# Optimization experiments

Measured on AMD Instinct MI355X. Metric: run time of the kernel, lower is better.

The kernel has to match this reference:

```python
import jax, jax.numpy as jnp
import numpy as np

TAU = 1.0 / 30.0
EPS = 1e-12  # matches torch F.normalize clamp_min eps


def _l2norm(x):
    n = jnp.sqrt(jnp.sum(x * x, axis=-1, keepdims=True))
    return x / jnp.maximum(n, EPS)


def setup_inputs() -> dict:
    key = jax.random.key(0)
    ks = jax.random.split(key, 6)
    L, B, D, KD = 4096, 4, 512, 128
    query = jax.random.normal(ks[0], (L, B, D), dtype=jnp.float32)
    k_in = jax.random.normal(ks[1], (L, B, D), dtype=jnp.float32)
    value = jax.random.normal(ks[2], (L, B, D), dtype=jnp.float32)
    # init: normal(0, sqrt(2/out_features)), zero bias
    WK_w = jax.random.normal(ks[3], (KD, D), dtype=jnp.float32) * np.sqrt(2.0 / KD)
    WK_b = jnp.zeros((KD,), dtype=jnp.float32)
    WV_w = jax.random.normal(ks[4], (D, D), dtype=jnp.float32) * np.sqrt(2.0 / D)
    WV_b = jnp.zeros((D,), dtype=jnp.float32)
    return {"query": query, "key": k_in, "value": value,
            "WK_w": WK_w, "WK_b": WK_b, "WV_w": WV_w, "WV_b": WV_b}


def reference(query, key, value, WK_w, WK_b, WV_w, WV_b):
    # query/key/value: [L, B, D]
    wk = _l2norm(key @ WK_w.T + WK_b)      # [Lk, B, KD]
    wq = _l2norm(query @ WK_w.T + WK_b)    # [Lq, B, KD]
    wv = value @ WV_w.T + WV_b             # [Lk, B, D]
    # cosine-similarity scores: [B, Lq, Lk]
    scores = jnp.einsum('qbk,sbk->bqs', wq, wk)
    affinity = jax.nn.softmax(scores / TAU, axis=-1)
    out = jnp.einsum('bqs,sbd->qbd', affinity, wv)  # [Lq, B, D]
    return out
```

## Files before the change

kernel.cpp:

```cpp
#include <hip/hip_runtime.h>

using bf16x8 = __attribute__((ext_vector_type(8))) short;
using u16x8  = __attribute__((ext_vector_type(8))) unsigned short;
using f32x4  = __attribute__((ext_vector_type(4))) float;
using f32x4v = __attribute__((ext_vector_type(4))) float;

__device__ inline unsigned short f2bf(float f) {
  unsigned int u = __builtin_bit_cast(unsigned int, f);
  return (unsigned short)((u + 0x7fffu + ((u >> 16) & 1u)) >> 16);
}

#define MFMA16(a, b, c) __builtin_amdgcn_mfma_f32_16x16x32_bf16((a), (b), (c), 0, 0, 0)

__device__ __forceinline__ void lds_barrier() {
  __builtin_amdgcn_sched_barrier(0);
  asm volatile("s_waitcnt lgkmcnt(0)" ::: "memory");
  __builtin_amdgcn_sched_barrier(0);
  __builtin_amdgcn_s_barrier();
  __builtin_amdgcn_sched_barrier(0);
}

#define LL 4096
#define NB 4
#define DD 512
#define KDIM 128

__device__ __forceinline__ void proj_qk_body(
    char* smem, int bid, const float* __restrict__ Xq, const float* __restrict__ Xk,
    const float* __restrict__ Wk, const float* __restrict__ bk,
    unsigned short* __restrict__ Outq, unsigned short* __restrict__ Outk)
{
  char* Xs = smem;
  char* Ws = smem + 16384;

  const int tid = threadIdx.x;
  const int w = tid >> 6, lane = tid & 63, lr = lane & 15, g = lane >> 4;
  const int sel = bid & 1;
  const float* X = sel ? Xk : Xq;
  unsigned short* Out = sel ? Outk : Outq;
  const int r0 = (bid >> 1) * 64;

  f32x4 acc[8];
  #pragma unroll
  for (int nt = 0; nt < 8; ++nt) acc[nt] = f32x4{0.f, 0.f, 0.f, 0.f};

  for (int kc = 0; kc < 4; ++kc) {
    if (kc) __syncthreads();
    #pragma unroll
    for (int p = 0; p < 4; ++p) {
      int j = tid + p * 256;
      int row = j >> 4, e0 = (j & 15) * 8;
      const float* src = X + (size_t)(r0 + row) * DD + kc * 128 + e0;
      f32x4v f0 = *reinterpret_cast<const f32x4v*>(src);
      f32x4v f1 = *reinterpret_cast<const f32x4v*>(src + 4);
      u16x8 v;
      #pragma unroll
      for (int e = 0; e < 4; ++e) { v[e] = f2bf(f0[e]); v[e + 4] = f2bf(f1[e]); }
      *reinterpret_cast<u16x8*>(Xs + row * 256 + ((e0 * 2) ^ ((row & 7) << 4))) = v;
    }
    #pragma unroll
    for (int p = 0; p < 8; ++p) {
      int j = tid + p * 256;
      int n = j >> 4, e0 = (j & 15) * 8;
      const float* src = Wk + (size_t)n * DD + kc * 128 + e0;
      f32x4v f0 = *reinterpret_cast<const f32x4v*>(src);
      f32x4v f1 = *reinterpret_cast<const f32x4v*>(src + 4);
      u16x8 v;
      #pragma unroll
      for (int e = 0; e < 4; ++e) { v[e] = f2bf(f0[e]); v[e + 4] = f2bf(f1[e]); }
      *reinterpret_cast<u16x8*>(Ws + n * 256 + ((e0 * 2) ^ ((n & 7) << 4))) = v;
    }
    __syncthreads();
    const int arow = w * 16 + lr;
    #pragma unroll
    for (int ks = 0; ks < 4; ++ks) {
      int oa = (ks * 64 + g * 16) ^ ((arow & 7) << 4);
      bf16x8 a = *reinterpret_cast<const bf16x8*>(Xs + arow * 256 + oa);
      #pragma unroll
      for (int nt = 0; nt < 8; ++nt) {
        int n = nt * 16 + lr;
        int ob = (ks * 64 + g * 16) ^ ((n & 7) << 4);
        bf16x8 bb = *reinterpret_cast<const bf16x8*>(Ws + n * 256 + ob);
        acc[nt] = MFMA16(a, bb, acc[nt]);
      }
    }
  }

  float bias[8];
  #pragma unroll
  for (int nt = 0; nt < 8; ++nt) bias[nt] = bk[nt * 16 + lr];
  #pragma unroll
  for (int nt = 0; nt < 8; ++nt)
    #pragma unroll
    for (int i = 0; i < 4; ++i) acc[nt][i] += bias[nt];

  f32x4 ss = f32x4{0.f, 0.f, 0.f, 0.f};
  #pragma unroll
  for (int nt = 0; nt < 8; ++nt)
    #pragma unroll
    for (int i = 0; i < 4; ++i) ss[i] += acc[nt][i] * acc[nt][i];
  #pragma unroll
  for (int m = 1; m < 16; m <<= 1) {
    #pragma unroll
    for (int i = 0; i < 4; ++i) ss[i] += __shfl_xor(ss[i], m);
  }
  float inv[4];
  #pragma unroll
  for (int i = 0; i < 4; ++i) inv[i] = 1.0f / fmaxf(sqrtf(ss[i]), 1e-12f);

  #pragma unroll
  for (int nt = 0; nt < 8; ++nt) {
    int c = nt * 16 + lr;
    #pragma unroll
    for (int i = 0; i < 4; ++i) {
      int r = r0 + w * 16 + g * 4 + i;
      int l = r >> 2, b = r & 3;
      Out[((size_t)(b * LL + l)) * KDIM + c] = f2bf(acc[nt][i] * inv[i]);
    }
  }
}

__device__ __forceinline__ void proj_v_body(
    char* smem, int bid, const float* __restrict__ X,
    const float* __restrict__ Wv, const float* __restrict__ bv,
    unsigned short* __restrict__ VtOut)
{
  char* Xs = smem;
  char* Ws = smem + 32768;

  const int tid = threadIdx.x;
  const int w = tid >> 6, lane = tid & 63, lr = lane & 15, g = lane >> 4;
  const int rb = bid >> 3, nb = bid & 7;
  const int r0 = rb * 256, d0 = nb * 64;

  f32x4 acc[4][4];
  #pragma unroll
  for (int rt = 0; rt < 4; ++rt)
    #pragma unroll
    for (int nt = 0; nt < 4; ++nt) acc[rt][nt] = f32x4{0.f, 0.f, 0.f, 0.f};

  for (int kc = 0; kc < 8; ++kc) {
    if (kc) __syncthreads();
    #pragma unroll
    for (int p = 0; p < 8; ++p) {
      int j = tid + p * 256;
      int row = j >> 3, e0 = (j & 7) * 8;
      const float* src = X + (size_t)(r0 + row) * DD + kc * 64 + e0;
      f32x4v f0 = *reinterpret_cast<const f32x4v*>(src);
      f32x4v f1 = *reinterpret_cast<const f32x4v*>(src + 4);
      u16x8 v;
      #pragma unroll
      for (int e = 0; e < 4; ++e) { v[e] = f2bf(f0[e]); v[e + 4] = f2bf(f1[e]); }
      *reinterpret_cast<u16x8*>(Xs + row * 128 + ((e0 * 2) ^ ((row & 7) << 4))) = v;
    }
    #pragma unroll
    for (int p = 0; p < 2; ++p) {
      int j = tid + p * 256;
      int n = j >> 3, e0 = (j & 7) * 8;
      const float* src = Wv + (size_t)(d0 + n) * DD + kc * 64 + e0;
      f32x4v f0 = *reinterpret_cast<const f32x4v*>(src);
      f32x4v f1 = *reinterpret_cast<const f32x4v*>(src + 4);
      u16x8 v;
      #pragma unroll
      for (int e = 0; e < 4; ++e) { v[e] = f2bf(f0[e]); v[e + 4] = f2bf(f1[e]); }
      *reinterpret_cast<u16x8*>(Ws + n * 128 + ((e0 * 2) ^ ((n & 7) << 4))) = v;
    }
    __syncthreads();
    #pragma unroll
    for (int ks = 0; ks < 2; ++ks) {
      bf16x8 a[4];
      #pragma unroll
      for (int rt = 0; rt < 4; ++rt) {
        int arow = w * 64 + rt * 16 + lr;
        a[rt] = *reinterpret_cast<const bf16x8*>(
            Xs + arow * 128 + ((ks * 64 + g * 16) ^ ((arow & 7) << 4)));
      }
      #pragma unroll
      for (int nt = 0; nt < 4; ++nt) {
        int n = nt * 16 + lr;
        bf16x8 bb = *reinterpret_cast<const bf16x8*>(
            Ws + n * 128 + ((ks * 64 + g * 16) ^ ((n & 7) << 4)));
        #pragma unroll
        for (int rt = 0; rt < 4; ++rt) acc[rt][nt] = MFMA16(a[rt], bb, acc[rt][nt]);
      }
    }
  }

  __syncthreads();
  float bias[4];
  #pragma unroll
  for (int nt = 0; nt < 4; ++nt) bias[nt] = bv[d0 + nt * 16 + lr];

  unsigned short* Ts = (unsigned short*)smem;
  #pragma unroll
  for (int rt = 0; rt < 4; ++rt)
    #pragma unroll
    for (int nt = 0; nt < 4; ++nt) {
      int dl = nt * 16 + lr;
      #pragma unroll
      for (int i = 0; i < 4; ++i) {
        int rl = w * 64 + rt * 16 + g * 4 + i;
        Ts[dl * 256 + (rl ^ ((dl & 31) << 1))] = f2bf(acc[rt][nt][i] + bias[nt]);
      }
    }
  __syncthreads();

  int bsel = tid >> 6, dl = tid & 63;
  int l0 = r0 >> 2;
  #pragma unroll
  for (int jj = 0; jj < 8; ++jj) {
    u16x8 v;
    #pragma unroll
    for (int e = 0; e < 8; ++e) {
      int rl = (jj * 8 + e) * 4 + bsel;
      v[e] = Ts[dl * 256 + (rl ^ ((dl & 31) << 1))];
    }
    *reinterpret_cast<u16x8*>(VtOut + ((size_t)(bsel * DD + d0 + dl)) * LL + l0 + jj * 8) = v;
  }
}

__global__ __launch_bounds__(256) void proj_all_kernel(
    const float* __restrict__ Xq, const float* __restrict__ Xk,
    const float* __restrict__ Xv,
    const float* __restrict__ Wk, const float* __restrict__ bk,
    const float* __restrict__ Wv, const float* __restrict__ bv,
    unsigned short* __restrict__ Outq, unsigned short* __restrict__ Outk,
    unsigned short* __restrict__ VtOut)
{
  __shared__ char smem[49152];
  const int bid = blockIdx.x;
  if (bid < 512) {
    proj_qk_body(smem, bid, Xq, Xk, Wk, bk, Outq, Outk);
  } else {
    proj_v_body(smem, bid - 512, Xv, Wv, bv, VtOut);
  }
}

#define QBLK 64
#define KBLK 64
#define NIT (LL / KBLK)

template<bool DOPV, bool TAIL>
__device__ __forceinline__ void attn_body(
    int tS, const unsigned short* __restrict__ Kp,
    const unsigned short* __restrict__ Vp,
    const char* kcur, char* knxt, const char* prd, char* pwr,
    const bf16x8 (&qf)[4], bf16x8 (&vst)[4][2],
    u16x8 (&kstW)[2], u16x8 (&kstL)[2],
    f32x4 (&acc)[4][4], float (&lsum)[4],
    int lr, int g, int w, int wq, int ws, int r0k, int c0k)
{
  const int tK2 = TAIL ? tS : tS + 2;
  const int tV1 = TAIL ? tS : tS + 1;

  {
    const unsigned short* src = Kp + ((size_t)(tK2 * KBLK + r0k)) * KDIM + c0k;
    kstL[0] = *reinterpret_cast<const u16x8*>(src);
    kstL[1] = *reinterpret_cast<const u16x8*>(src + 32 * KDIM);
  }

  bf16x8 kb[2][4];
  #pragma unroll
  for (int sch = 0; sch < 2; ++sch) {
    int sr = ws * 32 + sch * 16 + lr;
    #pragma unroll
    for (int kc = 0; kc < 4; ++kc)
      kb[sch][kc] = *reinterpret_cast<const bf16x8*>(
          kcur + sr * 256 + ((kc * 64 + g * 16) ^ ((sr & 7) << 4)));
  }
  bf16x8 pf[2][2];
  if (DOPV) {
    #pragma unroll
    for (int qt = 0; qt < 2; ++qt) {
      int q = qt * 16 + lr, swz = (q & 7) << 4;
      pf[qt][0] = *reinterpret_cast<const bf16x8*>(prd + q * 128 + ((g * 16) ^ swz));
      pf[qt][1] = *reinterpret_cast<const bf16x8*>(prd + q * 128 + ((64 + g * 16) ^ swz));
    }
  }
  __builtin_amdgcn_sched_barrier(0);
  asm volatile("s_waitcnt lgkmcnt(0)" ::: "memory");
  __builtin_amdgcn_sched_barrier(0);

  f32x4 s0 = f32x4{0.f, 0.f, 0.f, 0.f};
  f32x4 s1 = f32x4{0.f, 0.f, 0.f, 0.f};
  __builtin_amdgcn_s_setprio(1);
  #pragma unroll
  for (int kc = 0; kc < 4; ++kc) {
    s0 = MFMA16(qf[kc], kb[0][kc], s0);
    s1 = MFMA16(qf[kc], kb[1][kc], s1);
  }
  if (DOPV) {
    #pragma unroll
    for (int qt = 0; qt < 2; ++qt)
      #pragma unroll
      for (int ch = 0; ch < 4; ++ch) {
        acc[qt][ch] = MFMA16(pf[qt][0], vst[ch][0], acc[qt][ch]);
        acc[qt][ch] = MFMA16(pf[qt][1], vst[ch][1], acc[qt][ch]);
      }
  }
  __builtin_amdgcn_s_setprio(0);

  if (DOPV) {
    bf16x8 pf2[2][2];
    #pragma unroll
    for (int qt = 0; qt < 2; ++qt) {
      int q = (qt + 2) * 16 + lr, swz = (q & 7) << 4;
      pf2[qt][0] = *reinterpret_cast<const bf16x8*>(prd + q * 128 + ((g * 16) ^ swz));
      pf2[qt][1] = *reinterpret_cast<const bf16x8*>(prd + q * 128 + ((64 + g * 16) ^ swz));
    }
    __builtin_amdgcn_sched_barrier(0);
    asm volatile("s_waitcnt lgkmcnt(0)" ::: "memory");
    __builtin_amdgcn_sched_barrier(0);
    __builtin_amdgcn_s_setprio(1);
    #pragma unroll
    for (int qt = 0; qt < 2; ++qt)
      #pragma unroll
      for (int ch = 0; ch < 4; ++ch) {
        acc[qt + 2][ch] = MFMA16(pf2[qt][0], vst[ch][0], acc[qt + 2][ch]);
        acc[qt + 2][ch] = MFMA16(pf2[qt][1], vst[ch][1], acc[qt + 2][ch]);
      }
    __builtin_amdgcn_s_setprio(0);
  }

  #pragma unroll
  for (int ch = 0; ch < 4; ++ch)
    #pragma unroll
    for (int sc = 0; sc < 2; ++sc)
      vst[ch][sc] = *reinterpret_cast<const bf16x8*>(
          Vp + (size_t)(w * 64 + ch * 16 + lr) * LL + tV1 * KBLK + sc * 32 + g * 8);

  const int sr0 = ws * 32 + lr, sr1 = sr0 + 16;
  #pragma unroll
  for (int i = 0; i < 4; ++i) {
    float p0 = exp2f(fmaf(s0[i], 43.280851f, -44.723546f));
    float p1 = exp2f(fmaf(s1[i], 43.280851f, -44.723546f));
    lsum[i] += p0 + p1;
    int q = wq * 16 + g * 4 + i, swz = (q & 7) << 4;
    *(unsigned short*)(pwr + q * 128 + ((sr0 * 2) ^ swz)) = f2bf(p0);
    *(unsigned short*)(pwr + q * 128 + ((sr1 * 2) ^ swz)) = f2bf(p1);
  }

  {
    int swz = (r0k & 7) << 4;
    *reinterpret_cast<u16x8*>(knxt + r0k * 256 + ((c0k * 2) ^ swz)) = kstW[0];
    *reinterpret_cast<u16x8*>(knxt + (r0k + 32) * 256 + ((c0k * 2) ^ swz)) = kstW[1];
  }
  lds_barrier();
}

__global__ __launch_bounds__(512, 2) void attn_kernel(
    const unsigned short* __restrict__ Qn, const unsigned short* __restrict__ Kn,
    const unsigned short* __restrict__ Vt, float* __restrict__ Out)
{
  __shared__ char smem[49664];
  char* Ks0 = smem;
  char* Ks1 = smem + 16384;
  char* Ps0 = smem + 32768;
  char* Ps1 = smem + 40960;
  float* Ls = (float*)(smem + 49152);

  const int tid = threadIdx.x;
  const int w = tid >> 6, lane = tid & 63, lr = lane & 15, g = lane >> 4;
  const int wq = w & 3, ws = w >> 2;
  const int r0k = tid >> 4, c0k = (tid & 15) * 8;

  const int bid = blockIdx.x;
  const int b = (bid & 7) >> 1;
  const int tile = ((bid >> 3) << 1) | (bid & 1);
  const int q0 = tile * QBLK;

  const unsigned short* Kp = Kn + (size_t)b * LL * KDIM;
  const unsigned short* Vp = Vt + (size_t)b * DD * LL;

  bf16x8 qf[4];
  {
    const unsigned short* qp = Qn + ((size_t)(b * LL + q0 + wq * 16 + lr)) * KDIM + g * 8;
    #pragma unroll
    for (int kc = 0; kc < 4; ++kc)
      qf[kc] = *reinterpret_cast<const bf16x8*>(qp + kc * 32);
  }

  f32x4 acc[4][4];
  #pragma unroll
  for (int qt = 0; qt < 4; ++qt)
    #pragma unroll
    for (int ch = 0; ch < 4; ++ch) acc[qt][ch] = f32x4{0.f, 0.f, 0.f, 0.f};
  float lsum[4] = {0.f, 0.f, 0.f, 0.f};

  bf16x8 vstA[4][2], vstB[4][2];
  u16x8 kstE[2], kstO[2];

  {
    u16x8 k0 = *reinterpret_cast<const u16x8*>(Kp + (size_t)r0k * KDIM + c0k);
    u16x8 k1 = *reinterpret_cast<const u16x8*>(Kp + (size_t)(r0k + 32) * KDIM + c0k);
    int swz = (r0k & 7) << 4;
    *reinterpret_cast<u16x8*>(Ks0 + r0k * 256 + ((c0k * 2) ^ swz)) = k0;
    *reinterpret_cast<u16x8*>(Ks0 + (r0k + 32) * 256 + ((c0k * 2) ^ swz)) = k1;
    #pragma unroll
    for (int ch = 0; ch < 4; ++ch)
      #pragma unroll
      for (int sc = 0; sc < 2; ++sc)
        vstA[ch][sc] = *reinterpret_cast<const bf16x8*>(
            Vp + (size_t)(w * 64 + ch * 16 + lr) * LL + sc * 32 + g * 8);
    const unsigned short* src = Kp + ((size_t)(1 * KBLK + r0k)) * KDIM + c0k;
    kstO[0] = *reinterpret_cast<const u16x8*>(src);
    kstO[1] = *reinterpret_cast<const u16x8*>(src + 32 * KDIM);
  }
  __syncthreads();

  attn_body<false, false>(0, Kp, Vp, Ks0, Ks1, Ps1, Ps0, qf, vstB, kstO, kstE,
                          acc, lsum, lr, g, w, wq, ws, r0k, c0k);

  for (int t = 1; t < 63; t += 2) {
    attn_body<true, false>(t,     Kp, Vp, Ks1, Ks0, Ps0, Ps1, qf, vstA, kstE, kstO,
                           acc, lsum, lr, g, w, wq, ws, r0k, c0k);
    attn_body<true, false>(t + 1, Kp, Vp, Ks0, Ks1, Ps1, Ps0, qf, vstB, kstO, kstE,
                           acc, lsum, lr, g, w, wq, ws, r0k, c0k);
  }
  attn_body<true, true>(63, Kp, Vp, Ks1, Ks0, Ps0, Ps1, qf, vstA, kstE, kstO,
                        acc, lsum, lr, g, w, wq, ws, r0k, c0k);

  #pragma unroll
  for (int qt = 0; qt < 4; ++qt) {
    int q = qt * 16 + lr, swz = (q & 7) << 4;
    bf16x8 pa0 = *reinterpret_cast<const bf16x8*>(Ps1 + q * 128 + ((g * 16) ^ swz));
    bf16x8 pa1 = *reinterpret_cast<const bf16x8*>(Ps1 + q * 128 + ((64 + g * 16) ^ swz));
    #pragma unroll
    for (int ch = 0; ch < 4; ++ch) {
      acc[qt][ch] = MFMA16(pa0, vstB[ch][0], acc[qt][ch]);
      acc[qt][ch] = MFMA16(pa1, vstB[ch][1], acc[qt][ch]);
    }
  }

  #pragma unroll
  for (int m = 1; m < 16; m <<= 1) {
    #pragma unroll
    for (int i = 0; i < 4; ++i) lsum[i] += __shfl_xor(lsum[i], m);
  }
  if (lr == 0) {
    #pragma unroll
    for (int i = 0; i < 4; ++i) Ls[ws * 64 + wq * 16 + g * 4 + i] = lsum[i];
  }
  __syncthreads();

  #pragma unroll
  for (int qt = 0; qt < 4; ++qt) {
    float linv[4];
    #pragma unroll
    for (int i = 0; i < 4; ++i) {
      int q = qt * 16 + g * 4 + i;
      linv[i] = 1.0f / (Ls[q] + Ls[64 + q]);
    }
    #pragma unroll
    for (int ch = 0; ch < 4; ++ch) {
      int d = w * 64 + ch * 16 + lr;
      #pragma unroll
      for (int i = 0; i < 4; ++i) {
        int q = q0 + qt * 16 + g * 4 + i;
        Out[((size_t)q * NB + b) * DD + d] = acc[qt][ch][i] * linv[i];
      }
    }
  }
}

extern "C" void kernel_launch(void* const* d_in, const int* in_sizes, int n_in,
                              void* d_out, int out_size, void* d_ws, size_t ws_size,
                              hipStream_t stream) {
  const float* query = (const float*)d_in[0];
  const float* key   = (const float*)d_in[1];
  const float* value = (const float*)d_in[2];
  const float* WKw   = (const float*)d_in[3];
  const float* WKb   = (const float*)d_in[4];
  const float* WVw   = (const float*)d_in[5];
  const float* WVb   = (const float*)d_in[6];
  float* out = (float*)d_out;

  unsigned short* wqn = (unsigned short*)d_ws;
  unsigned short* wkn = wqn + (size_t)NB * LL * KDIM;
  unsigned short* vt  = wkn + (size_t)NB * LL * KDIM;

  proj_all_kernel<<<1024, 256, 0, stream>>>(query, key, value,
                                            WKw, WKb, WVw, WVb,
                                            wqn, wkn, vt);
  attn_kernel<<<256, 512, 0, stream>>>(wqn, wkn, vt, out);
}
```

Measured before the change: 209.5 us.

## Double attention key block to 128 and simplify the prefetch pipeline

Raises the key/value tile from 64 to 128 rows, so each main-loop iteration does twice the QK and PV MFMA work and the loop needs half as many LDS barriers. The K prefetch distance drops from two tiles to one, and the double-buffered V register staging becomes a single buffer that is reloaded after the PV MFMAs. LDS use roughly doubles to about 98 KB of dynamic shared memory, set through hipFuncSetAttribute. The trade-off is more registers per thread and less overlap of global loads with compute, which may expose memory latency.

```diff
diff --git a/kernel.cpp b/kernel.cpp
--- a/kernel.cpp
+++ b/kernel.cpp
@@ -237,113 +237,110 @@
 }
 
 #define QBLK 64
-#define KBLK 64
+#define KBLK 128
 #define NIT (LL / KBLK)
 
 template<bool DOPV, bool TAIL>
 __device__ __forceinline__ void attn_body(
-    int tS, const unsigned short* __restrict__ Kp,
+    int t, const unsigned short* __restrict__ Kp,
     const unsigned short* __restrict__ Vp,
     const char* kcur, char* knxt, const char* prd, char* pwr,
-    const bf16x8 (&qf)[4], bf16x8 (&vst)[4][2],
-    u16x8 (&kstW)[2], u16x8 (&kstL)[2],
+    const bf16x8 (&qf)[4], bf16x8 (&vst)[4][4], u16x8 (&kst)[4],
     f32x4 (&acc)[4][4], float (&lsum)[4],
     int lr, int g, int w, int wq, int ws, int r0k, int c0k)
 {
-  const int tK2 = TAIL ? tS : tS + 2;
-  const int tV1 = TAIL ? tS : tS + 1;
-
-  {
-    const unsigned short* src = Kp + ((size_t)(tK2 * KBLK + r0k)) * KDIM + c0k;
-    kstL[0] = *reinterpret_cast<const u16x8*>(src);
-    kstL[1] = *reinterpret_cast<const u16x8*>(src + 32 * KDIM);
-  }
-
-  bf16x8 kb[2][4];
-  #pragma unroll
-  for (int sch = 0; sch < 2; ++sch) {
-    int sr = ws * 32 + sch * 16 + lr;
+  const int tn = TAIL ? t : t + 1;
+
+  #pragma unroll
+  for (int j = 0; j < 4; ++j)
+    kst[j] = *reinterpret_cast<const u16x8*>(
+        Kp + ((size_t)(tn * KBLK + r0k + 32 * j)) * KDIM + c0k);
+
+  f32x4 sacc[4];
+  #pragma unroll
+  for (int st = 0; st < 4; ++st) {
+    const int sr = ws * 64 + st * 16 + lr;
+    bf16x8 kb[4];
     #pragma unroll
     for (int kc = 0; kc < 4; ++kc)
-      kb[sch][kc] = *reinterpret_cast<const bf16x8*>(
+      kb[kc] = *reinterpret_cast<const bf16x8*>(
           kcur + sr * 256 + ((kc * 64 + g * 16) ^ ((sr & 7) << 4)));
-  }
-  bf16x8 pf[2][2];
+    sacc[st] = f32x4{0.f, 0.f, 0.f, 0.f};
+    #pragma unroll
+    for (int kc = 0; kc < 4; ++kc) sacc[st] = MFMA16(qf[kc], kb[kc], sacc[st]);
+  }
+
+  #pragma unroll
+  for (int st = 0; st < 4; ++st) {
+    const int s = ws * 64 + st * 16 + lr;
+    #pragma unroll
+    for (int i = 0; i < 4; ++i) {
+      float p = exp2f(fmaf(sacc[st][i], 43.280851f, -44.723546f));
+      lsum[i] += p;
+      int q = wq * 16 + g * 4 + i;
+      *(unsigned short*)(pwr + q * 256 + ((s * 2) ^ ((q & 7) << 4))) = f2bf(p);
+    }
+  }
+
   if (DOPV) {
-    #pragma unroll
-    for (int qt = 0; qt < 2; ++qt) {
-      int q = qt * 16 + lr, swz = (q & 7) << 4;
-      pf[qt][0] = *reinterpret_cast<const bf16x8*>(prd + q * 128 + ((g * 16) ^ swz));
-      pf[qt][1] = *reinterpret_cast<const bf16x8*>(prd + q * 128 + ((64 + g * 16) ^ swz));
-    }
-  }
-  __builtin_amdgcn_sched_barrier(0);
-  asm volatile("s_waitcnt lgkmcnt(0)" ::: "memory");
-  __builtin_amdgcn_sched_barrier(0);
-
-  f32x4 s0 = f32x4{0.f, 0.f, 0.f, 0.f};
-  f32x4 s1 = f32x4{0.f, 0.f, 0.f, 0.f};
-  __builtin_amdgcn_s_setprio(1);
-  #pragma unroll
-  for (int kc = 0; kc < 4; ++kc) {
-    s0 = MFMA16(qf[kc], kb[0][kc], s0);
-    s1 = MFMA16(qf[kc], kb[1][kc], s1);
-  }
-  if (DOPV) {
-    #pragma unroll
-    for (int qt = 0; qt < 2; ++qt)
-      #pragma unroll
-      for (int ch = 0; ch < 4; ++ch) {
-        acc[qt][ch] = MFMA16(pf[qt][0], vst[ch][0], acc[qt][ch]);
-        acc[qt][ch] = MFMA16(pf[qt][1], vst[ch][1], acc[qt][ch]);
-      }
-  }
-  __builtin_amdgcn_s_setprio(0);
-
-  if (DOPV) {
-    bf16x8 pf2[2][2];
-    #pragma unroll
-    for (int qt = 0; qt < 2; ++qt) {
-      int q = (qt + 2) * 16 + lr, swz = (q & 7) << 4;
-      pf2[qt][0] = *reinterpret_cast<const bf16x8*>(prd + q * 128 + ((g * 16) ^ swz));
-      pf2[qt][1] = *reinterpret_cast<const bf16x8*>(prd + q * 128 + ((64 + g * 16) ^ swz));
-    }
-    __builtin_amdgcn_sched_barrier(0);
-    asm volatile("s_waitcnt lgkmcnt(0)" ::: "memory");
-    __builtin_amdgcn_sched_barrier(0);
-    __builtin_amdgcn_s_setprio(1);
-    #pragma unroll
-    for (int qt = 0; qt < 2; ++qt)
-      #pragma unroll
-      for (int ch = 0; ch < 4; ++ch) {
-        acc[qt + 2][ch] = MFMA16(pf2[qt][0], vst[ch][0], acc[qt + 2][ch]);
-        acc[qt + 2][ch] = MFMA16(pf2[qt][1], vst[ch][1], acc[qt + 2][ch]);
-      }
-    __builtin_amdgcn_s_setprio(0);
-  }
-
-  #pragma unroll
-  for (int ch = 0; ch < 4; ++ch)
-    #pragma unroll
-    for (int sc = 0; sc < 2; ++sc)
-      vst[ch][sc] = *reinterpret_cast<const bf16x8*>(
-          Vp + (size_t)(w * 64 + ch * 16 + lr) * LL + tV1 * KBLK + sc * 32 + g * 8);
-
-  const int sr0 = ws * 32 + lr, sr1 = sr0 + 16;
-  #pragma unroll
-  for (int i = 0; i < 4; ++i) {
-    float p0 = exp2f(fmaf(s0[i], 43.280851f, -44.723546f));
-    float p1 = exp2f(fmaf(s1[i], 43.280851f, -44.723546f));
-    lsum[i] += p0 + p1;
-    int q = wq * 16 + g * 4 + i, swz = (q & 7) << 4;
-    *(unsigned short*)(pwr + q * 128 + ((sr0 * 2) ^ swz)) = f2bf(p0);
-    *(unsigned short*)(pwr + q * 128 + ((sr1 * 2) ^ swz)) = f2bf(p1);
-  }
-
-  {
-    int swz = (r0k & 7) << 4;
-    *reinterpret_cast<u16x8*>(knxt + r0k * 256 + ((c0k * 2) ^ swz)) = kstW[0];
-    *reinterpret_cast<u16x8*>(knxt + (r0k + 32) * 256 + ((c0k * 2) ^ swz)) = kstW[1];
+    {
+      bf16x8 pf[2][4];
+      #pragma unroll
+      for (int qt = 0; qt < 2; ++qt) {
+        int q = qt * 16 + lr, swz = (q & 7) << 4;
+        #pragma unroll
+        for (int ks = 0; ks < 4; ++ks)
+          pf[qt][ks] = *reinterpret_cast<const bf16x8*>(
+              prd + q * 256 + ((ks * 64 + g * 16) ^ swz));
+      }
+      __builtin_amdgcn_sched_barrier(0);
+      asm volatile("s_waitcnt lgkmcnt(0)" ::: "memory");
+      __builtin_amdgcn_sched_barrier(0);
+      __builtin_amdgcn_s_setprio(1);
+      #pragma unroll
+      for (int qt = 0; qt < 2; ++qt)
+        #pragma unroll
+        for (int ch = 0; ch < 4; ++ch)
+          #pragma unroll
+          for (int ks = 0; ks < 4; ++ks)
+            acc[qt][ch] = MFMA16(pf[qt][ks], vst[ch][ks], acc[qt][ch]);
+      __builtin_amdgcn_s_setprio(0);
+    }
+    {
+      bf16x8 pf[2][4];
+      #pragma unroll
+      for (int qt = 0; qt < 2; ++qt) {
+        int q = (qt + 2) * 16 + lr, swz = (q & 7) << 4;
+        #pragma unroll
+        for (int ks = 0; ks < 4; ++ks)
+          pf[qt][ks] = *reinterpret_cast<const bf16x8*>(
+              prd + q * 256 + ((ks * 64 + g * 16) ^ swz));
+      }
+      __builtin_amdgcn_sched_barrier(0);
+      asm volatile("s_waitcnt lgkmcnt(0)" ::: "memory");
+      __builtin_amdgcn_sched_barrier(0);
+      __builtin_amdgcn_s_setprio(1);
+      #pragma unroll
+      for (int qt = 0; qt < 2; ++qt)
+        #pragma unroll
+        for (int ch = 0; ch < 4; ++ch)
+          #pragma unroll
+          for (int ks = 0; ks < 4; ++ks)
+            acc[qt + 2][ch] = MFMA16(pf[qt][ks], vst[ch][ks], acc[qt + 2][ch]);
+      __builtin_amdgcn_s_setprio(0);
+    }
+    #pragma unroll
+    for (int ch = 0; ch < 4; ++ch)
+      #pragma unroll
+      for (int ks = 0; ks < 4; ++ks)
+        vst[ch][ks] = *reinterpret_cast<const bf16x8*>(
+            Vp + (size_t)(w * 64 + ch * 16 + lr) * LL + t * KBLK + ks * 32 + g * 8);
+  }
+
+  #pragma unroll
+  for (int j = 0; j < 4; ++j) {
+    int row = r0k + 32 * j;
+    *reinterpret_cast<u16x8*>(knxt + row * 256 + ((c0k * 2) ^ ((row & 7) << 4))) = kst[j];
   }
   lds_barrier();
 }
@@ -352,12 +349,12 @@
     const unsigned short* __restrict__ Qn, const unsigned short* __restrict__ Kn,
     const unsigned short* __restrict__ Vt, float* __restrict__ Out)
 {
-  __shared__ char smem[49664];
+  extern __shared__ char smem[];
   char* Ks0 = smem;
-  char* Ks1 = smem + 16384;
-  char* Ps0 = smem + 32768;
-  char* Ps1 = smem + 40960;
-  float* Ls = (float*)(smem + 49152);
+  char* Ks1 = smem + 32768;
+  char* Ps0 = smem + 65536;
+  char* Ps1 = smem + 81920;
+  float* Ls = (float*)(smem + 98304);
 
   const int tid = threadIdx.x;
   const int w = tid >> 6, lane = tid & 63, lr = lane & 15, g = lane >> 4;
@@ -387,49 +384,50 @@
     for (int ch = 0; ch < 4; ++ch) acc[qt][ch] = f32x4{0.f, 0.f, 0.f, 0.f};
   float lsum[4] = {0.f, 0.f, 0.f, 0.f};
 
-  bf16x8 vstA[4][2], vstB[4][2];
-  u16x8 kstE[2], kstO[2];
+  bf16x8 vst[4][4];
+  u16x8 kst[4];
 
   {
-    u16x8 k0 = *reinterpret_cast<const u16x8*>(Kp + (size_t)r0k * KDIM + c0k);
-    u16x8 k1 = *reinterpret_cast<const u16x8*>(Kp + (size_t)(r0k + 32) * KDIM + c0k);
-    int swz = (r0k & 7) << 4;
-    *reinterpret_cast<u16x8*>(Ks0 + r0k * 256 + ((c0k * 2) ^ swz)) = k0;
-    *reinterpret_cast<u16x8*>(Ks0 + (r0k + 32) * 256 + ((c0k * 2) ^ swz)) = k1;
+    #pragma unroll
+    for (int j = 0; j < 4; ++j) {
+      int row = r0k + 32 * j;
+      u16x8 v = *reinterpret_cast<const u16x8*>(Kp + (size_t)row * KDIM + c0k);
+      *reinterpret_cast<u16x8*>(Ks0 + row * 256 + ((c0k * 2) ^ ((row & 7) << 4))) = v;
+    }
     #pragma unroll
     for (int ch = 0; ch < 4; ++ch)
       #pragma unroll
-      for (int sc = 0; sc < 2; ++sc)
-        vstA[ch][sc] = *reinterpret_cast<const bf16x8*>(
-            Vp + (size_t)(w * 64 + ch * 16 + lr) * LL + sc * 32 + g * 8);
-    const unsigned short* src = Kp + ((size_t)(1 * KBLK + r0k)) * KDIM + c0k;
-    kstO[0] = *reinterpret_cast<const u16x8*>(src);
-    kstO[1] = *reinterpret_cast<const u16x8*>(src + 32 * KDIM);
+      for (int ks = 0; ks < 4; ++ks)
+        vst[ch][ks] = *reinterpret_cast<const bf16x8*>(
+            Vp + (size_t)(w * 64 + ch * 16 + lr) * LL + ks * 32 + g * 8);
   }
   __syncthreads();
 
-  attn_body<false, false>(0, Kp, Vp, Ks0, Ks1, Ps1, Ps0, qf, vstB, kstO, kstE,
+  attn_body<false, false>(0, Kp, Vp, Ks0, Ks1, Ps1, Ps0, qf, vst, kst,
                           acc, lsum, lr, g, w, wq, ws, r0k, c0k);
 
-  for (int t = 1; t < 63; t += 2) {
-    attn_body<true, false>(t,     Kp, Vp, Ks1, Ks0, Ps0, Ps1, qf, vstA, kstE, kstO,
+  for (int t = 1; t < 31; t += 2) {
+    attn_body<true, false>(t,     Kp, Vp, Ks1, Ks0, Ps0, Ps1, qf, vst, kst,
                            acc, lsum, lr, g, w, wq, ws, r0k, c0k);
-    attn_body<true, false>(t + 1, Kp, Vp, Ks0, Ks1, Ps1, Ps0, qf, vstB, kstO, kstE,
+    attn_body<true, false>(t + 1, Kp, Vp, Ks0, Ks1, Ps1, Ps0, qf, vst, kst,
                            acc, lsum, lr, g, w, wq, ws, r0k, c0k);
   }
-  attn_body<true, true>(63, Kp, Vp, Ks1, Ks0, Ps0, Ps1, qf, vstA, kstE, kstO,
+  attn_body<true, true>(31, Kp, Vp, Ks1, Ks0, Ps0, Ps1, qf, vst, kst,
                         acc, lsum, lr, g, w, wq, ws, r0k, c0k);
 
   #pragma unroll
   for (int qt = 0; qt < 4; ++qt) {
     int q = qt * 16 + lr, swz = (q & 7) << 4;
-    bf16x8 pa0 = *reinterpret_cast<const bf16x8*>(Ps1 + q * 128 + ((g * 16) ^ swz));
-    bf16x8 pa1 = *reinterpret_cast<const bf16x8*>(Ps1 + q * 128 + ((64 + g * 16) ^ swz));
-    #pragma unroll
-    for (int ch = 0; ch < 4; ++ch) {
-      acc[qt][ch] = MFMA16(pa0, vstB[ch][0], acc[qt][ch]);
-      acc[qt][ch] = MFMA16(pa1, vstB[ch][1], acc[qt][ch]);
-    }
+    bf16x8 pf[4];
+    #pragma unroll
+    for (int ks = 0; ks < 4; ++ks)
+      pf[ks] = *reinterpret_cast<const bf16x8*>(
+          Ps1 + q * 256 + ((ks * 64 + g * 16) ^ swz));
+    #pragma unroll
+    for (int ch = 0; ch < 4; ++ch)
+      #pragma unroll
+      for (int ks = 0; ks < 4; ++ks)
+        acc[qt][ch] = MFMA16(pf[ks], vst[ch][ks], acc[qt][ch]);
   }
 
   #pragma unroll
@@ -479,8 +477,15 @@
   unsigned short* wkn = wqn + (size_t)NB * LL * KDIM;
   unsigned short* vt  = wkn + (size_t)NB * LL * KDIM;
 
+  static bool attr_set = false;
+  if (!attr_set) {
+    hipFuncSetAttribute((const void*)attn_kernel,
+                        hipFuncAttributeMaxDynamicSharedMemorySize, 98816);
+    attr_set = true;
+  }
+
   proj_all_kernel<<<1024, 256, 0, stream>>>(query, key, value,
                                             WKw, WKb, WVw, WVb,
                                             wqn, wkn, vt);
-  attn_kernel<<<256, 512, 0, stream>>>(wqn, wkn, vt, out);
-}
+  attn_kernel<<<256, 512, 98816, stream>>>(wqn, wkn, vt, out);
+}
```

Result: slower. 275.7 us (+31.6%).
